# Performance work log

Measured on AMD Instinct MI355X. Metric: run time of the kernel, lower is better.

## Reference

```python
import jax, jax.numpy as jnp
import numpy as np

B, T, E, D = 64, 128, 4, 128
K = 4 * D  # ffn_hidden_dim
AUX_COEF = 0.01


def setup_inputs() -> dict:
    key = jax.random.key(0)
    ks = jax.random.split(key, 7)
    return {
        "x": jax.random.normal(ks[0], (B, T, D), dtype=jnp.float32),
        "expert_w1": jax.random.normal(ks[1], (T, E, D, K), dtype=jnp.float32) * 0.02,
        "expert_b1": jnp.zeros((T, E, K), dtype=jnp.float32),
        "expert_w2": jax.random.normal(ks[2], (T, E, K, D), dtype=jnp.float32) * 0.02,
        "expert_b2": jnp.zeros((T, E, D), dtype=jnp.float32),
        # router_train nn.Linear(D, E): store as [D, E] plus bias [E]
        "router_w": jax.random.normal(ks[3], (D, E), dtype=jnp.float32) * (1.0 / np.sqrt(D)),
        "router_b": jax.random.normal(ks[4], (E,), dtype=jnp.float32) * 0.01,
    }


def reference(x, expert_w1, expert_b1, expert_w2, expert_b2, router_w, router_b):
    # training=True path with use_relu_routing=True
    router_logits = jnp.einsum("btd,de->bte", x, router_w) + router_b  # [B,T,E]
    gates = jax.nn.relu(router_logits)
    gates = gates / (gates.sum(axis=-1, keepdims=True) + 1e-9)

    # per-token, per-expert 2-layer FFN
    hidden = jnp.einsum("btd,tedk->btek", x, expert_w1) + expert_b1  # [B,T,E,K]
    hidden = jax.nn.gelu(hidden, approximate=False)  # torch F.gelu default = exact erf
    expert_outputs = jnp.einsum("btek,tekd->bted", hidden, expert_w2) + expert_b2  # [B,T,E,D]

    output = (expert_outputs * gates[..., None]).sum(axis=2)  # [B,T,D]
    aux_loss = AUX_COEF * gates.sum() / (x.shape[0] * x.shape[1])
    return output, aux_loss
```

## Files before the change

kernel.cpp:

```cpp
#include <hip/hip_runtime.h>
#include <hip/hip_bf16.h>

#define NB 64
#define NT 128
#define NE 4
#define ND 128
#define NK 512

typedef __attribute__((ext_vector_type(8))) short bf16x8;
typedef __attribute__((ext_vector_type(4))) float f32x4;

__device__ __forceinline__ short f2bf(float f) {
    union { float f; unsigned u; } v; v.f = f;
    unsigned r = v.u + 0x7FFFu + ((v.u >> 16) & 1u);
    return (short)(r >> 16);
}

__device__ __forceinline__ float gelu_erf(float x) {
    return 0.5f * x * (1.0f + erff(x * 0.70710678118654752f));
}

__global__ __launch_bounds__(256, 2)
void moe_main(const float* __restrict__ x,
              const float* __restrict__ w1,
              const float* __restrict__ b1,
              const float* __restrict__ w2,
              const float* __restrict__ b2,
              const float* __restrict__ rw,
              const float* __restrict__ rb,
              float* __restrict__ out,
              float* __restrict__ ws,
              int use_ws)
{
    const int blk  = blockIdx.x;
    const int t    = blk >> 2;
    const int e    = blk & 3;
    const int tid  = threadIdx.x;
    const int lane = tid & 63;
    const int wave = tid >> 6;
    const int l15  = lane & 15;
    const int l4   = lane >> 4;

    __shared__ short Hs[NB][NK + 8];
    __shared__ float gate_s[NB];

    if (tid < NB) {
        const int b = tid;
        const float* xr = x + (b * NT + t) * ND;
        float l0 = rb[0], l1 = rb[1], l2 = rb[2], l3 = rb[3];
        #pragma unroll 8
        for (int d = 0; d < ND; ++d) {
            const float xv = xr[d];
            const float* w = rw + d * NE;
            l0 += xv * w[0]; l1 += xv * w[1]; l2 += xv * w[2]; l3 += xv * w[3];
        }
        l0 = fmaxf(l0, 0.f); l1 = fmaxf(l1, 0.f); l2 = fmaxf(l2, 0.f); l3 = fmaxf(l3, 0.f);
        const float s   = l0 + l1 + l2 + l3;
        const float inv = 1.f / (s + 1e-9f);
        const float ge  = (e == 0) ? l0 : (e == 1) ? l1 : (e == 2) ? l2 : l3;
        gate_s[b] = ge * inv;
        if (e == 0) {
            float aux = s * inv;
            #pragma unroll
            for (int off = 32; off > 0; off >>= 1) aux += __shfl_down(aux, off);
            if (lane == 0) atomicAdd(out + NB * NT * ND, aux * (0.01f / (NB * NT)));
        }
    }
    __syncthreads();

    const float* W1 = w1 + (size_t)((t * NE + e) * ND) * NK;
    const float* B1 = b1 + (t * NE + e) * NK;
    const int n0 = wave * 128;

    f32x4 acc[4][8];
    #pragma unroll
    for (int m = 0; m < 4; ++m)
        #pragma unroll
        for (int n = 0; n < 8; ++n) acc[m][n] = (f32x4){0.f, 0.f, 0.f, 0.f};

    #pragma unroll
    for (int ks = 0; ks < 4; ++ks) {
        const int d0 = ks * 32 + l4 * 8;
        bf16x8 afr[4];
        #pragma unroll
        for (int m = 0; m < 4; ++m) {
            const int b = m * 16 + l15;
            const float* xp = x + (b * NT + t) * ND + d0;
            const float4 u = *(const float4*)(xp);
            const float4 v = *(const float4*)(xp + 4);
            bf16x8 a;
            a[0] = f2bf(u.x); a[1] = f2bf(u.y); a[2] = f2bf(u.z); a[3] = f2bf(u.w);
            a[4] = f2bf(v.x); a[5] = f2bf(v.y); a[6] = f2bf(v.z); a[7] = f2bf(v.w);
            afr[m] = a;
        }
        #pragma unroll
        for (int nt = 0; nt < 8; ++nt) {
            const int n = n0 + nt * 16 + l15;
            const float* wp = W1 + (size_t)d0 * NK + n;
            bf16x8 bfr;
            #pragma unroll
            for (int j = 0; j < 8; ++j) bfr[j] = f2bf(wp[(size_t)j * NK]);
            #pragma unroll
            for (int m = 0; m < 4; ++m)
                acc[m][nt] = __builtin_amdgcn_mfma_f32_16x16x32_bf16(afr[m], bfr, acc[m][nt], 0, 0, 0);
        }
    }

    #pragma unroll
    for (int nt = 0; nt < 8; ++nt) {
        const int n = n0 + nt * 16 + l15;
        const float bb = B1[n];
        #pragma unroll
        for (int m = 0; m < 4; ++m) {
            const int row = m * 16 + l4 * 4;
            #pragma unroll
            for (int r = 0; r < 4; ++r) {
                const float h = acc[m][nt][r] + bb;
                Hs[row + r][n] = f2bf(gelu_erf(h));
            }
        }
    }
    __syncthreads();

    const float* W2 = w2 + (size_t)((t * NE + e) * NK) * ND;
    const float* B2 = b2 + (t * NE + e) * ND;
    const int c0 = wave * 32;

    f32x4 acc2[4][2];
    #pragma unroll
    for (int m = 0; m < 4; ++m)
        #pragma unroll
        for (int n = 0; n < 2; ++n) acc2[m][n] = (f32x4){0.f, 0.f, 0.f, 0.f};

    #pragma unroll 4
    for (int ks = 0; ks < 16; ++ks) {
        const int k0 = ks * 32 + l4 * 8;
        bf16x8 afr[4];
        #pragma unroll
        for (int m = 0; m < 4; ++m)
            afr[m] = *(const bf16x8*)(&Hs[m * 16 + l15][k0]);
        #pragma unroll
        for (int nt = 0; nt < 2; ++nt) {
            const int c = c0 + nt * 16 + l15;
            const float* wp = W2 + (size_t)k0 * ND + c;
            bf16x8 bfr;
            #pragma unroll
            for (int j = 0; j < 8; ++j) bfr[j] = f2bf(wp[(size_t)j * ND]);
            #pragma unroll
            for (int m = 0; m < 4; ++m)
                acc2[m][nt] = __builtin_amdgcn_mfma_f32_16x16x32_bf16(afr[m], bfr, acc2[m][nt], 0, 0, 0);
        }
    }

    #pragma unroll
    for (int nt = 0; nt < 2; ++nt) {
        const int c = c0 + nt * 16 + l15;
        const float bb = B2[c];
        #pragma unroll
        for (int m = 0; m < 4; ++m) {
            #pragma unroll
            for (int r = 0; r < 4; ++r) {
                const int b = m * 16 + l4 * 4 + r;
                const float v = (acc2[m][nt][r] + bb) * gate_s[b];
                if (use_ws) ws[(size_t)(e * NB * NT + b * NT + t) * ND + c] = v;
                else        atomicAdd(out + (size_t)(b * NT + t) * ND + c, v);
            }
        }
    }
}

__global__ __launch_bounds__(256)
void moe_reduce(const float* __restrict__ ws, float* __restrict__ out)
{
    const int i = blockIdx.x * blockDim.x + threadIdx.x;
    const int stride = NB * NT * ND / 4;
    const float4* w = (const float4*)ws;
    const float4 a = w[i];
    const float4 b = w[i + stride];
    const float4 c = w[i + 2 * stride];
    const float4 d = w[i + 3 * stride];
    float4 r;
    r.x = a.x + b.x + c.x + d.x;
    r.y = a.y + b.y + c.y + d.y;
    r.z = a.z + b.z + c.z + d.z;
    r.w = a.w + b.w + c.w + d.w;
    ((float4*)out)[i] = r;
}

extern "C" void kernel_launch(void* const* d_in, const int* in_sizes, int n_in,
                              void* d_out, int out_size, void* d_ws, size_t ws_size,
                              hipStream_t stream) {
    const float* x  = (const float*)d_in[0];
    const float* w1 = (const float*)d_in[1];
    const float* b1 = (const float*)d_in[2];
    const float* w2 = (const float*)d_in[3];
    const float* b2 = (const float*)d_in[4];
    const float* rw = (const float*)d_in[5];
    const float* rb = (const float*)d_in[6];
    float* out = (float*)d_out;

    const size_t ws_need = (size_t)NE * NB * NT * ND * sizeof(float);
    const int use_ws = (ws_size >= ws_need) ? 1 : 0;

    if (use_ws) {
        hipMemsetAsync(out + NB * NT * ND, 0, sizeof(float), stream);
    } else {
        hipMemsetAsync(d_out, 0, (size_t)(NB * NT * ND + 1) * sizeof(float), stream);
    }

    moe_main<<<NT * NE, 256, 0, stream>>>(x, w1, b1, w2, b2, rw, rb, out,
                                          (float*)d_ws, use_ws);
    if (use_ws) {
        moe_reduce<<<(NB * NT * ND / 4) / 256, 256, 0, stream>>>((const float*)d_ws, out);
    }
}
```

Baseline: 76.28 us.

## Split batch across two blocks per (t,e) and hoist router into separate kernel

```diff
diff --git a/kernel.cpp b/kernel.cpp
--- a/kernel.cpp
+++ b/kernel.cpp
@@ -6,6 +6,7 @@
 #define NE 4
 #define ND 128
 #define NK 512
+#define MH 32
 
 typedef __attribute__((ext_vector_type(8))) short bf16x8;
 typedef __attribute__((ext_vector_type(4))) float f32x4;
@@ -20,71 +21,100 @@
     return 0.5f * x * (1.0f + erff(x * 0.70710678118654752f));
 }
 
-__global__ __launch_bounds__(256, 2)
+__global__ __launch_bounds__(256)
+void moe_gates(const float* __restrict__ x,
+               const float* __restrict__ rw,
+               const float* __restrict__ rb,
+               float* __restrict__ gates_ws,
+               float* __restrict__ aux_partial)
+{
+    const int tid  = threadIdx.x;
+    const int lane = tid & 63;
+    const int wave = tid >> 6;
+    __shared__ float waux[4];
+
+    const float4 rw0 = *(const float4*)(rw + lane * 4);
+    const float4 rw1 = *(const float4*)(rw + (64 + lane) * 4);
+    const float4 rbv = *(const float4*)rb;
+
+    float aux = 0.f;
+    #pragma unroll
+    for (int i = 0; i < 4; ++i) {
+        const int tok = (blockIdx.x * 4 + wave) * 4 + i;
+        const float x0 = x[tok * ND + lane];
+        const float x1 = x[tok * ND + 64 + lane];
+        float p0 = x0 * rw0.x + x1 * rw1.x;
+        float p1 = x0 * rw0.y + x1 * rw1.y;
+        float p2 = x0 * rw0.z + x1 * rw1.z;
+        float p3 = x0 * rw0.w + x1 * rw1.w;
+        #pragma unroll
+        for (int off = 32; off > 0; off >>= 1) {
+            p0 += __shfl_xor(p0, off);
+            p1 += __shfl_xor(p1, off);
+            p2 += __shfl_xor(p2, off);
+            p3 += __shfl_xor(p3, off);
+        }
+        if (lane == 0) {
+            p0 = fmaxf(p0 + rbv.x, 0.f);
+            p1 = fmaxf(p1 + rbv.y, 0.f);
+            p2 = fmaxf(p2 + rbv.z, 0.f);
+            p3 = fmaxf(p3 + rbv.w, 0.f);
+            const float s   = p0 + p1 + p2 + p3;
+            const float inv = 1.f / (s + 1e-9f);
+            float4 g; g.x = p0 * inv; g.y = p1 * inv; g.z = p2 * inv; g.w = p3 * inv;
+            *(float4*)(gates_ws + tok * NE) = g;
+            aux += s * inv;
+        }
+    }
+    if (lane == 0) waux[wave] = aux;
+    __syncthreads();
+    if (tid == 0)
+        aux_partial[blockIdx.x] = waux[0] + waux[1] + waux[2] + waux[3];
+}
+
+__global__ __launch_bounds__(256, 4)
 void moe_main(const float* __restrict__ x,
               const float* __restrict__ w1,
               const float* __restrict__ b1,
               const float* __restrict__ w2,
               const float* __restrict__ b2,
-              const float* __restrict__ rw,
-              const float* __restrict__ rb,
-              float* __restrict__ out,
-              float* __restrict__ ws,
-              int use_ws)
+              const float* __restrict__ gates_ws,
+              float* __restrict__ ws)
 {
-    const int blk  = blockIdx.x;
-    const int t    = blk >> 2;
-    const int e    = blk & 3;
+    const int bid  = blockIdx.x;
+    const int h    = bid >> 9;
+    const int s    = bid & 511;
+    const int t    = s >> 2;
+    const int e    = s & 3;
     const int tid  = threadIdx.x;
     const int lane = tid & 63;
     const int wave = tid >> 6;
     const int l15  = lane & 15;
     const int l4   = lane >> 4;
 
-    __shared__ short Hs[NB][NK + 8];
-    __shared__ float gate_s[NB];
-
-    if (tid < NB) {
-        const int b = tid;
-        const float* xr = x + (b * NT + t) * ND;
-        float l0 = rb[0], l1 = rb[1], l2 = rb[2], l3 = rb[3];
-        #pragma unroll 8
-        for (int d = 0; d < ND; ++d) {
-            const float xv = xr[d];
-            const float* w = rw + d * NE;
-            l0 += xv * w[0]; l1 += xv * w[1]; l2 += xv * w[2]; l3 += xv * w[3];
-        }
-        l0 = fmaxf(l0, 0.f); l1 = fmaxf(l1, 0.f); l2 = fmaxf(l2, 0.f); l3 = fmaxf(l3, 0.f);
-        const float s   = l0 + l1 + l2 + l3;
-        const float inv = 1.f / (s + 1e-9f);
-        const float ge  = (e == 0) ? l0 : (e == 1) ? l1 : (e == 2) ? l2 : l3;
-        gate_s[b] = ge * inv;
-        if (e == 0) {
-            float aux = s * inv;
-            #pragma unroll
-            for (int off = 32; off > 0; off >>= 1) aux += __shfl_down(aux, off);
-            if (lane == 0) atomicAdd(out + NB * NT * ND, aux * (0.01f / (NB * NT)));
-        }
-    }
-    __syncthreads();
+    __shared__ short Hs[MH][NK + 8];
+    __shared__ float gate_s[MH];
+
+    if (tid < MH)
+        gate_s[tid] = gates_ws[((h * MH + tid) * NT + t) * NE + e];
 
     const float* W1 = w1 + (size_t)((t * NE + e) * ND) * NK;
     const float* B1 = b1 + (t * NE + e) * NK;
     const int n0 = wave * 128;
 
-    f32x4 acc[4][8];
-    #pragma unroll
-    for (int m = 0; m < 4; ++m)
+    f32x4 acc[2][8];
+    #pragma unroll
+    for (int m = 0; m < 2; ++m)
         #pragma unroll
         for (int n = 0; n < 8; ++n) acc[m][n] = (f32x4){0.f, 0.f, 0.f, 0.f};
 
     #pragma unroll
     for (int ks = 0; ks < 4; ++ks) {
         const int d0 = ks * 32 + l4 * 8;
-        bf16x8 afr[4];
-        #pragma unroll
-        for (int m = 0; m < 4; ++m) {
-            const int b = m * 16 + l15;
+        bf16x8 afr[2];
+        #pragma unroll
+        for (int m = 0; m < 2; ++m) {
+            const int b = h * MH + m * 16 + l15;
             const float* xp = x + (b * NT + t) * ND + d0;
             const float4 u = *(const float4*)(xp);
             const float4 v = *(const float4*)(xp + 4);
@@ -101,7 +131,7 @@
             #pragma unroll
             for (int j = 0; j < 8; ++j) bfr[j] = f2bf(wp[(size_t)j * NK]);
             #pragma unroll
-            for (int m = 0; m < 4; ++m)
+            for (int m = 0; m < 2; ++m)
                 acc[m][nt] = __builtin_amdgcn_mfma_f32_16x16x32_bf16(afr[m], bfr, acc[m][nt], 0, 0, 0);
         }
     }
@@ -111,12 +141,12 @@
         const int n = n0 + nt * 16 + l15;
         const float bb = B1[n];
         #pragma unroll
-        for (int m = 0; m < 4; ++m) {
+        for (int m = 0; m < 2; ++m) {
             const int row = m * 16 + l4 * 4;
             #pragma unroll
             for (int r = 0; r < 4; ++r) {
-                const float h = acc[m][nt][r] + bb;
-                Hs[row + r][n] = f2bf(gelu_erf(h));
+                const float hh = acc[m][nt][r] + bb;
+                Hs[row + r][n] = f2bf(gelu_erf(hh));
             }
         }
     }
@@ -126,18 +156,18 @@
     const float* B2 = b2 + (t * NE + e) * ND;
     const int c0 = wave * 32;
 
-    f32x4 acc2[4][2];
-    #pragma unroll
-    for (int m = 0; m < 4; ++m)
+    f32x4 acc2[2][2];
+    #pragma unroll
+    for (int m = 0; m < 2; ++m)
         #pragma unroll
         for (int n = 0; n < 2; ++n) acc2[m][n] = (f32x4){0.f, 0.f, 0.f, 0.f};
 
     #pragma unroll 4
     for (int ks = 0; ks < 16; ++ks) {
         const int k0 = ks * 32 + l4 * 8;
-        bf16x8 afr[4];
-        #pragma unroll
-        for (int m = 0; m < 4; ++m)
+        bf16x8 afr[2];
+        #pragma unroll
+        for (int m = 0; m < 2; ++m)
             afr[m] = *(const bf16x8*)(&Hs[m * 16 + l15][k0]);
         #pragma unroll
         for (int nt = 0; nt < 2; ++nt) {
@@ -147,7 +177,7 @@
             #pragma unroll
             for (int j = 0; j < 8; ++j) bfr[j] = f2bf(wp[(size_t)j * ND]);
             #pragma unroll
-            for (int m = 0; m < 4; ++m)
+            for (int m = 0; m < 2; ++m)
                 acc2[m][nt] = __builtin_amdgcn_mfma_f32_16x16x32_bf16(afr[m], bfr, acc2[m][nt], 0, 0, 0);
         }
     }
@@ -157,20 +187,22 @@
         const int c = c0 + nt * 16 + l15;
         const float bb = B2[c];
         #pragma unroll
-        for (int m = 0; m < 4; ++m) {
+        for (int m = 0; m < 2; ++m) {
             #pragma unroll
             for (int r = 0; r < 4; ++r) {
-                const int b = m * 16 + l4 * 4 + r;
-                const float v = (acc2[m][nt][r] + bb) * gate_s[b];
-                if (use_ws) ws[(size_t)(e * NB * NT + b * NT + t) * ND + c] = v;
-                else        atomicAdd(out + (size_t)(b * NT + t) * ND + c, v);
+                const int bl = m * 16 + l4 * 4 + r;
+                const int b  = h * MH + bl;
+                const float v = (acc2[m][nt][r] + bb) * gate_s[bl];
+                ws[(size_t)(e * NB * NT + b * NT + t) * ND + c] = v;
             }
         }
     }
 }
 
 __global__ __launch_bounds__(256)
-void moe_reduce(const float* __restrict__ ws, float* __restrict__ out)
+void moe_reduce(const float* __restrict__ ws,
+                const float* __restrict__ aux_partial,
+                float* __restrict__ out)
 {
     const int i = blockIdx.x * blockDim.x + threadIdx.x;
     const int stride = NB * NT * ND / 4;
@@ -185,6 +217,165 @@
     r.z = a.z + b.z + c.z + d.z;
     r.w = a.w + b.w + c.w + d.w;
     ((float4*)out)[i] = r;
+
+    if (blockIdx.x == 0) {
+        const int tid = threadIdx.x;
+        float s = aux_partial[tid] + aux_partial[tid + 256];
+        #pragma unroll
+        for (int off = 32; off > 0; off >>= 1) s += __shfl_xor(s, off);
+        __shared__ float wsum[4];
+        if ((tid & 63) == 0) wsum[tid >> 6] = s;
+        __syncthreads();
+        if (tid == 0)
+            out[NB * NT * ND] = (wsum[0] + wsum[1] + wsum[2] + wsum[3]) *
+                                (0.01f / (NB * NT));
+    }
+}
+
+__global__ __launch_bounds__(256, 2)
+void moe_main_fb(const float* __restrict__ x,
+                 const float* __restrict__ w1,
+                 const float* __restrict__ b1,
+                 const float* __restrict__ w2,
+                 const float* __restrict__ b2,
+                 const float* __restrict__ rw,
+                 const float* __restrict__ rb,
+                 float* __restrict__ out)
+{
+    const int blk  = blockIdx.x;
+    const int t    = blk >> 2;
+    const int e    = blk & 3;
+    const int tid  = threadIdx.x;
+    const int lane = tid & 63;
+    const int wave = tid >> 6;
+    const int l15  = lane & 15;
+    const int l4   = lane >> 4;
+
+    __shared__ short Hs[NB][NK + 8];
+    __shared__ float gate_s[NB];
+
+    if (tid < NB) {
+        const int b = tid;
+        const float* xr = x + (b * NT + t) * ND;
+        float l0 = rb[0], l1 = rb[1], l2 = rb[2], l3 = rb[3];
+        #pragma unroll 8
+        for (int d = 0; d < ND; ++d) {
+            const float xv = xr[d];
+            const float* w = rw + d * NE;
+            l0 += xv * w[0]; l1 += xv * w[1]; l2 += xv * w[2]; l3 += xv * w[3];
+        }
+        l0 = fmaxf(l0, 0.f); l1 = fmaxf(l1, 0.f); l2 = fmaxf(l2, 0.f); l3 = fmaxf(l3, 0.f);
+        const float ss  = l0 + l1 + l2 + l3;
+        const float inv = 1.f / (ss + 1e-9f);
+        const float ge  = (e == 0) ? l0 : (e == 1) ? l1 : (e == 2) ? l2 : l3;
+        gate_s[b] = ge * inv;
+        if (e == 0) {
+            float aux = ss * inv;
+            #pragma unroll
+            for (int off = 32; off > 0; off >>= 1) aux += __shfl_down(aux, off);
+            if (lane == 0) atomicAdd(out + NB * NT * ND, aux * (0.01f / (NB * NT)));
+        }
+    }
+    __syncthreads();
+
+    const float* W1 = w1 + (size_t)((t * NE + e) * ND) * NK;
+    const float* B1 = b1 + (t * NE + e) * NK;
+    const int n0 = wave * 128;
+
+    f32x4 acc[4][8];
+    #pragma unroll
+    for (int m = 0; m < 4; ++m)
+        #pragma unroll
+        for (int n = 0; n < 8; ++n) acc[m][n] = (f32x4){0.f, 0.f, 0.f, 0.f};
+
+    #pragma unroll
+    for (int ks = 0; ks < 4; ++ks) {
+        const int d0 = ks * 32 + l4 * 8;
+        bf16x8 afr[4];
+        #pragma unroll
+        for (int m = 0; m < 4; ++m) {
+            const int b = m * 16 + l15;
+            const float* xp = x + (b * NT + t) * ND + d0;
+            const float4 u = *(const float4*)(xp);
+            const float4 v = *(const float4*)(xp + 4);
+            bf16x8 a;
+            a[0] = f2bf(u.x); a[1] = f2bf(u.y); a[2] = f2bf(u.z); a[3] = f2bf(u.w);
+            a[4] = f2bf(v.x); a[5] = f2bf(v.y); a[6] = f2bf(v.z); a[7] = f2bf(v.w);
+            afr[m] = a;
+        }
+        #pragma unroll
+        for (int nt = 0; nt < 8; ++nt) {
+            const int n = n0 + nt * 16 + l15;
+            const float* wp = W1 + (size_t)d0 * NK + n;
+            bf16x8 bfr;
+            #pragma unroll
+            for (int j = 0; j < 8; ++j) bfr[j] = f2bf(wp[(size_t)j * NK]);
+            #pragma unroll
+            for (int m = 0; m < 4; ++m)
+                acc[m][nt] = __builtin_amdgcn_mfma_f32_16x16x32_bf16(afr[m], bfr, acc[m][nt], 0, 0, 0);
+        }
+    }
+
+    #pragma unroll
+    for (int nt = 0; nt < 8; ++nt) {
+        const int n = n0 + nt * 16 + l15;
+        const float bb = B1[n];
+        #pragma unroll
+        for (int m = 0; m < 4; ++m) {
+            const int row = m * 16 + l4 * 4;
+            #pragma unroll
+            for (int r = 0; r < 4; ++r) {
+                const float hh = acc[m][nt][r] + bb;
+                Hs[row + r][n] = f2bf(gelu_erf(hh));
+            }
+        }
+    }
+    __syncthreads();
+
+    const float* W2 = w2 + (size_t)((t * NE + e) * NK) * ND;
+    const float* B2 = b2 + (t * NE + e) * ND;
+    const int c0 = wave * 32;
+
+    f32x4 acc2[4][2];
+    #pragma unroll
+    for (int m = 0; m < 4; ++m)
+        #pragma unroll
+        for (int n = 0; n < 2; ++n) acc2[m][n] = (f32x4){0.f, 0.f, 0.f, 0.f};
+
+    #pragma unroll 4
+    for (int ks = 0; ks < 16; ++ks) {
+        const int k0 = ks * 32 + l4 * 8;
+        bf16x8 afr[4];
+        #pragma unroll
+        for (int m = 0; m < 4; ++m)
+            afr[m] = *(const bf16x8*)(&Hs[m * 16 + l15][k0]);
+        #pragma unroll
+        for (int nt = 0; nt < 2; ++nt) {
+            const int c = c0 + nt * 16 + l15;
+            const float* wp = W2 + (size_t)k0 * ND + c;
+            bf16x8 bfr;
+            #pragma unroll
+            for (int j = 0; j < 8; ++j) bfr[j] = f2bf(wp[(size_t)j * ND]);
+            #pragma unroll
+            for (int m = 0; m < 4; ++m)
+                acc2[m][nt] = __builtin_amdgcn_mfma_f32_16x16x32_bf16(afr[m], bfr, acc2[m][nt], 0, 0, 0);
+        }
+    }
+
+    #pragma unroll
+    for (int nt = 0; nt < 2; ++nt) {
+        const int c = c0 + nt * 16 + l15;
+        const float bb = B2[c];
+        #pragma unroll
+        for (int m = 0; m < 4; ++m) {
+            #pragma unroll
+            for (int r = 0; r < 4; ++r) {
+                const int b = m * 16 + l4 * 4 + r;
+                const float v = (acc2[m][nt][r] + bb) * gate_s[b];
+                atomicAdd(out + (size_t)(b * NT + t) * ND + c, v);
+            }
+        }
+    }
 }
 
 extern "C" void kernel_launch(void* const* d_in, const int* in_sizes, int n_in,
@@ -199,18 +390,21 @@
     const float* rb = (const float*)d_in[6];
     float* out = (float*)d_out;
 
-    const size_t ws_need = (size_t)NE * NB * NT * ND * sizeof(float);
-    const int use_ws = (ws_size >= ws_need) ? 1 : 0;
-
-    if (use_ws) {
-        hipMemsetAsync(out + NB * NT * ND, 0, sizeof(float), stream);
+    const size_t contrib_elems = (size_t)NE * NB * NT * ND;
+    const size_t gates_elems   = (size_t)NB * NT * NE;
+    const size_t aux_elems     = 512;
+    const size_t ws_need = (contrib_elems + gates_elems + aux_elems) * sizeof(float);
+
+    if (ws_size >= ws_need) {
+        float* contrib = (float*)d_ws;
+        float* gates   = contrib + contrib_elems;
+        float* auxp    = gates + gates_elems;
+
+        moe_gates<<<512, 256, 0, stream>>>(x, rw, rb, gates, auxp);
+        moe_main<<<NT * NE * 2, 256, 0, stream>>>(x, w1, b1, w2, b2, gates, contrib);
+        moe_reduce<<<(NB * NT * ND / 4) / 256, 256, 0, stream>>>(contrib, auxp, out);
     } else {
         hipMemsetAsync(d_out, 0, (size_t)(NB * NT * ND + 1) * sizeof(float), stream);
-    }
-
-    moe_main<<<NT * NE, 256, 0, stream>>>(x, w1, b1, w2, b2, rw, rb, out,
-                                          (float*)d_ws, use_ws);
-    if (use_ws) {
-        moe_reduce<<<(NB * NT * ND / 4) / 256, 256, 0, stream>>>((const float*)d_ws, out);
-    }
-}
+        moe_main_fb<<<NT * NE, 256, 0, stream>>>(x, w1, b1, w2, b2, rw, rb, out);
+    }
+}
```

Result: slower. 84.74 us (+11.1%).
